# Optimization experiments

Measured on AMD Instinct MI355X. Metric: run time of the kernel, lower is better.

Reference implementation:

```python
import jax, jax.numpy as jnp
import numpy as np

N_STACK = 12
ZERO_OFFSET = 0.001
EPS = 1e-8  # torch cosine_similarity eps


def cos_sim_vec_batch(a, b):
    """torch.cosine_similarity(a[None], b, dim=1): a [V], b [B,V] -> [B]."""
    na = jnp.maximum(jnp.sqrt(jnp.sum(a * a)), EPS)
    nb = jnp.maximum(jnp.sqrt(jnp.sum(b * b, axis=-1)), EPS)
    return (b @ a) / (na * nb)


def setup_inputs() -> dict:
    key = jax.random.key(0)
    k1, k2, k3, k4 = jax.random.split(key, 4)
    B, S, V = 64, 256, 2048
    return {
        "x": jax.random.normal(k1, (B, S, V), dtype=jnp.float32),
        "latch_init": jax.random.normal(k2, (B, V), dtype=jnp.float32),
        "should_pop": jax.random.normal(k3, (V,), dtype=jnp.float32),
        "sharpen_pointer": jnp.ones((1,), dtype=jnp.float32) * 5.0,
        "latch_enable": jax.random.normal(k4, (V,), dtype=jnp.float32) * 0.01,
    }


def reference(x, latch_init, should_pop, sharpen_pointer, latch_enable):
    B, S, V = x.shape
    sharpen = sharpen_pointer[0]
    # Stack state: stack [B, N, V] filled with zero_offset, pointer one-hot at slot 0.
    stack0 = jnp.full((B, N_STACK, V), ZERO_OFFSET, dtype=x.dtype)
    pointer0 = jnp.zeros((B, N_STACK), dtype=x.dtype).at[:, 0].set(1.0)

    def step(carry, inp):
        stack, pointer, latch = carry
        # per-step latch gating -> pop strength (dropout p=0.02 is identity in eval)
        pop = jax.nn.elu(cos_sim_vec_batch(should_pop, latch))  # [B]
        push = 1.0 - pop
        nop = jnp.zeros_like(pop)
        # sharpen the pointer, read the value that would be popped
        psharp = jax.nn.softmax(pointer * sharpen, axis=1)           # [B, N]
        pop_val = jnp.einsum('bnv,bn->bv', stack, psharp)
        # push branch: advance pointer, write value at new top
        push_p = jnp.roll(psharp, 1, axis=1)
        push_stack = stack * (1.0 - push_p[..., None]) + inp[:, None, :] * push_p[..., None]
        # pop branch: erase top back to zero_offset, retreat pointer
        pop_p = jnp.roll(psharp, -1, axis=1)
        pop_stack = stack * (1.0 - psharp[..., None]) + ZERO_OFFSET * psharp[..., None]
        # superposition of the three ops weighted by (push, pop, nop)
        new_stack = (push[:, None, None] * push_stack
                     + pop[:, None, None] * pop_stack
                     + nop[:, None, None] * stack)
        new_pointer = (push[:, None] * push_p
                       + pop[:, None] * pop_p
                       + nop[:, None] * psharp)
        # read stack top, gate by pop strength
        top = jnp.einsum('bnv,bn->bv', new_stack, new_pointer)      # [B, V]
        out = pop[:, None] * top
        # DataLatch update: interp by cosine sim of enable param with enable input
        e = cos_sim_vec_batch(latch_enable, inp)                     # [B]
        new_latch = (1.0 - e)[:, None] * latch + e[:, None] * inp
        return (new_stack, new_pointer, new_latch), (out, new_latch, pop, top)

    x_t = jnp.swapaxes(x, 0, 1)  # [S, B, V]
    _, (outs, latches, pops, tops) = jax.lax.scan(step, (stack0, pointer0, latch_init), x_t)
    outputs = jnp.swapaxes(outs, 0, 1)       # [B, S, V]
    latch_states = jnp.swapaxes(latches, 0, 1)
    pops_out = jnp.swapaxes(pops, 0, 1)       # [B, S]
    stack_tops = jnp.swapaxes(tops, 0, 1)
    return outputs, latch_states, pops_out, stack_tops
```

## Files before the change

kernel.cpp:

```cpp
#include <hip/hip_runtime.h>
#include <math.h>

#define B_ 64
#define S_ 256
#define V_ 2048
#define NS 12
#define ZOFF 0.001f
#define EPSF 1e-8f
#define EPS2 1e-16f
#define NCHS 32

#define WS_NSP2 0
#define WS_D0   64
#define WS_N0   128
#define WS_E    256
#define WS_R    (WS_E + B_*S_)
#define WS_NX2  (WS_R + B_*S_)
#define WS_H    (WS_NX2 + B_*S_)
#define WS_COEF (WS_H + B_*NCHS*S_*4)

typedef float f32x4 __attribute__((ext_vector_type(4)));

template<int CTRL>
__device__ __forceinline__ float dpp_mov(float x) {
    return __int_as_float(__builtin_amdgcn_update_dpp(
        0, __float_as_int(x), CTRL, 0xf, 0xf, true));
}

__device__ __forceinline__ float row16_sum(float x) {
    x += dpp_mov<0x121>(x);
    x += dpp_mov<0x122>(x);
    x += dpp_mov<0x124>(x);
    x += dpp_mov<0x128>(x);
    return x;
}

__device__ __forceinline__ float wave_sum64_fast(float x) {
    x = row16_sum(x);
    x += __shfl_xor(x, 16);
    x += __shfl_xor(x, 32);
    return x;
}

__device__ __forceinline__ void ntstore4(float* p, f32x4 v) {
    __builtin_nontemporal_store(v, (f32x4*)p);
}

__global__ void __launch_bounds__(256) k_e(const float* __restrict__ x,
                                           const float* __restrict__ le,
                                           const float* __restrict__ sp,
                                           const float* __restrict__ l0,
                                           float* __restrict__ ws) {
    int blk = blockIdx.x;
    int tid = threadIdx.x;
    int wave = tid >> 6, lane = tid & 63;
    __shared__ float red4[4][4];
    if (blk >= B_ * S_) {
        int nb = blk - B_ * S_;
        float a = 0.f, b = 0.f;
        if (nb == 0) {
            for (int i = tid; i < V_; i += 256) { float y = sp[i]; a += y * y; }
        } else {
            const float* lr = l0 + (size_t)(nb - 1) * V_;
            for (int i = tid; i < V_; i += 256) {
                float l = lr[i], s = sp[i];
                a += s * l; b += l * l;
            }
        }
        a = wave_sum64_fast(a); b = wave_sum64_fast(b);
        if (lane == 0) { red4[wave][0] = a; red4[wave][1] = b; }
        __syncthreads();
        if (tid == 0) {
            float s0 = red4[0][0] + red4[1][0] + red4[2][0] + red4[3][0];
            float s1 = red4[0][1] + red4[1][1] + red4[2][1] + red4[3][1];
            if (nb == 0) ws[WS_NSP2] = s0;
            else { ws[WS_D0 + nb - 1] = s0; ws[WS_N0 + nb - 1] = s1; }
        }
        return;
    }
    int bt = blk;
    const float4* xb = (const float4*)(x + (size_t)bt * V_);
    const float4* le4 = (const float4*)le;
    const float4* sp4 = (const float4*)sp;
    float dot = 0.f, nx = 0.f, rr = 0.f, nle = 0.f;
#pragma unroll
    for (int k = 0; k < 2; k++) {
        int i = tid + k * 256;
        float4 xv = xb[i], lv = le4[i], sv = sp4[i];
        dot += xv.x * lv.x + xv.y * lv.y + xv.z * lv.z + xv.w * lv.w;
        nx  += xv.x * xv.x + xv.y * xv.y + xv.z * xv.z + xv.w * xv.w;
        rr  += xv.x * sv.x + xv.y * sv.y + xv.z * sv.z + xv.w * sv.w;
        nle += lv.x * lv.x + lv.y * lv.y + lv.z * lv.z + lv.w * lv.w;
    }
    dot = wave_sum64_fast(dot); nx = wave_sum64_fast(nx);
    rr = wave_sum64_fast(rr);   nle = wave_sum64_fast(nle);
    if (lane == 0) {
        red4[wave][0] = dot; red4[wave][1] = nx;
        red4[wave][2] = rr;  red4[wave][3] = nle;
    }
    __syncthreads();
    if (tid == 0) {
        float d  = red4[0][0] + red4[1][0] + red4[2][0] + red4[3][0];
        float n  = red4[0][1] + red4[1][1] + red4[2][1] + red4[3][1];
        float r  = red4[0][2] + red4[1][2] + red4[2][2] + red4[3][2];
        float nl = red4[0][3] + red4[1][3] + red4[2][3] + red4[3][3];
        ws[WS_E + bt]   = d * __frsqrt_rn(fmaxf(nl, EPS2)) * __frsqrt_rn(fmaxf(n, EPS2));
        ws[WS_R + bt]   = r;
        ws[WS_NX2 + bt] = n;
    }
}

__global__ void __launch_bounds__(64) k_latch(const float* __restrict__ x,
                        const float* __restrict__ latch_init,
                        float* __restrict__ latch_out,
                        float* __restrict__ ws) {
    int c = blockIdx.x, b = blockIdx.y;
    int lane = threadIdx.x;
    int v = c * 64 + lane;

    __shared__ float se[S_];
    for (int t = lane; t < S_; t += 64) se[t] = ws[WS_E + b * S_ + t];
    __syncthreads();

    float latch = latch_init[(size_t)b * V_ + v];
    const float* xb = x + (size_t)b * S_ * V_ + v;
    float* lo = latch_out + (size_t)b * S_ * V_ + v;
    float* hpp = ws + WS_H + (size_t)(b * NCHS + c) * S_ * 4;
    bool hwr = (lane & 15) == 0;
    int hq = lane >> 4;

    auto step = [&](int t, float xv, float e) {
        float rs = row16_sum(latch * xv);
        if (hwr) hpp[t * 4 + hq] = rs;
        latch = fmaf(e, xv - latch, latch);
        __builtin_nontemporal_store(latch, lo + (size_t)t * V_);
    };

    float xc[8]; float ec[8];
#pragma unroll
    for (int k = 0; k < 8; k++) { xc[k] = xb[(size_t)k * V_]; ec[k] = se[k]; }
    for (int t = 0; t < S_; t += 8) {
        float y[8], f[8];
        if (t + 8 < S_) {
#pragma unroll
            for (int k = 0; k < 8; k++) {
                y[k] = xb[(size_t)(t + 8 + k) * V_];
                f[k] = se[t + 8 + k];
            }
        } else {
#pragma unroll
            for (int k = 0; k < 8; k++) { y[k] = 0.f; f[k] = 0.f; }
        }
#pragma unroll
        for (int k = 0; k < 8; k++) step(t + k, xc[k], ec[k]);
#pragma unroll
        for (int k = 0; k < 8; k++) { xc[k] = y[k]; ec[k] = f[k]; }
    }
}

template<bool UP>
__device__ __forceinline__ void ptr_fused(int lane, float kq, float inv_nsp,
                                          float d, float n,
                                          const float* __restrict__ se_,
                                          const float* __restrict__ sr_,
                                          const float* __restrict__ snx_,
                                          const float* __restrict__ sh,
                                          float* __restrict__ coef,
                                          float* __restrict__ pops_b) {
    bool act = lane < NS, is0 = (lane == 0), is11 = (lane == 11);
    bool wr = lane <= NS;
    float p = is0 ? 1.f : 0.f;

    float e8[8], r8[8], h8[8], x8[8];
#pragma unroll
    for (int k = 0; k < 8; k++) {
        e8[k] = se_[k]; r8[k] = sr_[k]; h8[k] = sh[k]; x8[k] = snx_[k];
    }
    for (int t = 0; t < S_; t += 8) {
        float e9[8], r9[8], h9[8], x9[8];
        if (t + 8 < S_) {
#pragma unroll
            for (int k = 0; k < 8; k++) {
                e9[k] = se_[t + 8 + k]; r9[k] = sr_[t + 8 + k];
                h9[k] = sh[t + 8 + k];  x9[k] = snx_[t + 8 + k];
            }
        } else {
#pragma unroll
            for (int k = 0; k < 8; k++) { e9[k] = r9[k] = h9[k] = x9[k] = 0.f; }
        }
#pragma unroll
        for (int k = 0; k < 8; k++) {
            float cs = d * inv_nsp * __frsqrt_rn(fmaxf(n, EPS2));
            float pop = cs > 0.f ? cs : __expf(cs) - 1.f;
            float push = 1.f - pop;
            float ez = act ? exp2f(p * kq) : 0.f;
            float s = row16_sum(ez);
            float psh = ez * __frcp_rn(s);
            float fm = UP ? dpp_mov<0x12F>(psh) : dpp_mov<0x121>(psh);
            float fp = UP ? dpp_mov<0x121>(psh) : dpp_mov<0x12F>(psh);
            float wm = UP ? dpp_mov<0x12B>(psh) : dpp_mov<0x125>(psh);
            float wp = UP ? dpp_mov<0x125>(psh) : dpp_mov<0x12B>(psh);
            float push_p = is0  ? wm : fm;
            float pop_p  = is11 ? wp : fp;
            float bb = push * push_p;
            float cc = pop * psh;
            float a  = 1.f - bb - cc;
            float pnew = fmaf(pop, pop_p, bb);
            float4 cv = act ? make_float4(a, bb, cc * ZOFF, pnew)
                            : make_float4(pop, 0.f, 0.f, 0.f);
            if (wr) *(float4*)(coef + (size_t)((t + k) * 13 + lane) * 4) = cv;
            if (lane == 0) pops_b[t + k] = pop;
            p = pnew;
            float e = e8[k], om = 1.f - e;
            d = fmaf(om, d, e * r8[k]);
            n = fmaf(om * om, n, fmaf(2.f * e * om, h8[k], e * e * x8[k]));
        }
#pragma unroll
        for (int k = 0; k < 8; k++) { e8[k] = e9[k]; r8[k] = r9[k]; h8[k] = h9[k]; x8[k] = x9[k]; }
    }
}

__global__ void __launch_bounds__(64) k_ptr(const float* __restrict__ sharpen_ptr,
                                            float* __restrict__ ws,
                                            float* __restrict__ pops_out) {
    int b = blockIdx.x, lane = threadIdx.x;
    __shared__ float sh[S_], se_[S_], sr_[S_], snx_[S_];
    const float4* hp4 = (const float4*)(ws + WS_H) + (size_t)b * NCHS * S_;
    for (int t = lane; t < S_; t += 64) {
        float h = 0.f;
#pragma unroll
        for (int c = 0; c < NCHS; c++) {
            float4 vv = hp4[(size_t)c * S_ + t];
            h += (vv.x + vv.y) + (vv.z + vv.w);
        }
        sh[t] = h;
        se_[t]  = ws[WS_E + b * S_ + t];
        sr_[t]  = ws[WS_R + b * S_ + t];
        snx_[t] = ws[WS_NX2 + b * S_ + t];
    }
    __syncthreads();

    float kq = sharpen_ptr[0] * 1.44269504f;
    float inv_nsp = 1.f / fmaxf(sqrtf(ws[WS_NSP2]), EPSF);
    float d0 = ws[WS_D0 + b];
    float n0 = ws[WS_N0 + b];
    float* coef = ws + WS_COEF + (size_t)b * S_ * 13 * 4;
    float* pops_b = pops_out + (size_t)b * S_;

    float pw = dpp_mov<0x121>((float)lane);
    bool up = (__builtin_amdgcn_readlane(__float_as_int(pw), 0) == __float_as_int(1.0f));
    if (up) ptr_fused<true>(lane, kq, inv_nsp, d0, n0, se_, sr_, snx_, sh, coef, pops_b);
    else    ptr_fused<false>(lane, kq, inv_nsp, d0, n0, se_, sr_, snx_, sh, coef, pops_b);
}

__global__ void __launch_bounds__(128) k_stack(const float* __restrict__ x,
                                               const float* __restrict__ ws,
                                               float* __restrict__ outputs,
                                               float* __restrict__ tops) {
    int b = blockIdx.y, ch = blockIdx.x;
    int tid = threadIdx.x;
    __shared__ float sc[S_ * 52];
    const float4* cb4 = (const float4*)(ws + WS_COEF + (size_t)b * S_ * 52);
    float4* sc4 = (float4*)sc;
    for (int i = tid; i < S_ * 13; i += 128) sc4[i] = cb4[i];
    __syncthreads();

    int v = ch * 512 + tid * 4;
    const float* xp = x + (size_t)b * S_ * V_ + v;
    float* op = outputs + (size_t)b * S_ * V_ + v;
    float* tp = tops + (size_t)b * S_ * V_ + v;

    f32x4 st[NS];
#pragma unroll
    for (int n = 0; n < NS; n++) st[n] = (f32x4){ZOFF, ZOFF, ZOFF, ZOFF};

    auto dstep = [&](int t, f32x4 xv) {
        const float* cf = &sc[t * 52];
        f32x4 top = (f32x4){0.f, 0.f, 0.f, 0.f};
#pragma unroll
        for (int n = 0; n < NS; n++) {
            float4 c4 = *(const float4*)(cf + n * 4);
            f32x4 bx;
            bx.x = fmaf(c4.y, xv.x, c4.z);
            bx.y = fmaf(c4.y, xv.y, c4.z);
            bx.z = fmaf(c4.y, xv.z, c4.z);
            bx.w = fmaf(c4.y, xv.w, c4.z);
            st[n].x = fmaf(c4.x, st[n].x, bx.x);
            st[n].y = fmaf(c4.x, st[n].y, bx.y);
            st[n].z = fmaf(c4.x, st[n].z, bx.z);
            st[n].w = fmaf(c4.x, st[n].w, bx.w);
            top.x = fmaf(c4.w, st[n].x, top.x);
            top.y = fmaf(c4.w, st[n].y, top.y);
            top.z = fmaf(c4.w, st[n].z, top.z);
            top.w = fmaf(c4.w, st[n].w, top.w);
        }
        float pop = cf[48];
        ntstore4(tp + (size_t)t * V_, top);
        f32x4 ot = {pop * top.x, pop * top.y, pop * top.z, pop * top.w};
        ntstore4(op + (size_t)t * V_, ot);
    };

    f32x4 xc[8];
#pragma unroll
    for (int k = 0; k < 8; k++) xc[k] = *(const f32x4*)(xp + (size_t)k * V_);
    for (int t = 0; t < S_; t += 8) {
        f32x4 y[8];
        if (t + 8 < S_) {
#pragma unroll
            for (int k = 0; k < 8; k++) y[k] = *(const f32x4*)(xp + (size_t)(t + 8 + k) * V_);
        } else {
#pragma unroll
            for (int k = 0; k < 8; k++) y[k] = (f32x4){0.f, 0.f, 0.f, 0.f};
        }
#pragma unroll
        for (int k = 0; k < 8; k++) dstep(t + k, xc[k]);
#pragma unroll
        for (int k = 0; k < 8; k++) xc[k] = y[k];
    }
}

extern "C" void kernel_launch(void* const* d_in, const int* in_sizes, int n_in,
                              void* d_out, int out_size, void* d_ws, size_t ws_size,
                              hipStream_t stream) {
    const float* x           = (const float*)d_in[0];
    const float* latch_init  = (const float*)d_in[1];
    const float* should_pop  = (const float*)d_in[2];
    const float* sharpen_ptr = (const float*)d_in[3];
    const float* latch_en    = (const float*)d_in[4];

    float* out = (float*)d_out;
    const size_t BSV = (size_t)B_ * S_ * V_;
    float* outputs      = out;
    float* latch_states = out + BSV;
    float* pops         = out + 2 * BSV;
    float* tops         = out + 2 * BSV + (size_t)B_ * S_;
    float* ws = (float*)d_ws;

    k_e<<<B_ * S_ + 1 + B_, 256, 0, stream>>>(x, latch_en, should_pop, latch_init, ws);
    k_latch<<<dim3(NCHS, B_), 64, 0, stream>>>(x, latch_init, latch_states, ws);
    k_ptr<<<B_, 64, 0, stream>>>(sharpen_ptr, ws, pops);
    k_stack<<<dim3(4, B_), 128, 0, stream>>>(x, ws, outputs, tops);
}
```

Before: 202.2 us.

## Fuse pointer recurrence into stack scan kernel, recomputing coefficients per wave

Removes the separate pointer kernel and the workspace coefficient buffer. Each wave now computes the pointer/pop recurrence step-by-step and writes coefficients to a small double-buffered LDS slot consumed by its own stack scan. This eliminates a launch, the serial single-wave-per-batch phase, and the global round trip for coefficients. In exchange, the serial chain is recomputed redundantly by all 8 waves per batch and lengthens each streaming step's dependency chain.

```diff
diff --git a/kernel.cpp b/kernel.cpp
--- a/kernel.cpp
+++ b/kernel.cpp
@@ -17,7 +17,6 @@
 #define WS_R    (WS_E + B_*S_)
 #define WS_NX2  (WS_R + B_*S_)
 #define WS_H    (WS_NX2 + B_*S_)
-#define WS_COEF (WS_H + B_*NCHS*S_*4)
 
 typedef float f32x4 __attribute__((ext_vector_type(4)));
 
@@ -159,140 +158,67 @@
 }
 
 template<bool UP>
-__device__ __forceinline__ void ptr_fused(int lane, float kq, float inv_nsp,
-                                          float d, float n,
-                                          const float* __restrict__ se_,
-                                          const float* __restrict__ sr_,
-                                          const float* __restrict__ snx_,
-                                          const float* __restrict__ sh,
-                                          float* __restrict__ coef,
-                                          float* __restrict__ pops_b) {
+__device__ __forceinline__ void fused_loop(
+    int lane, float kq, float inv_nsp, float d, float n,
+    const float* __restrict__ sh, const float* __restrict__ se_,
+    const float* __restrict__ sr_, const float* __restrict__ snx_,
+    float* __restrict__ slot0, float* __restrict__ slot1,
+    const float* __restrict__ xp, float* __restrict__ op,
+    float* __restrict__ tp, float* __restrict__ pops_b, bool wrpops)
+{
     bool act = lane < NS, is0 = (lane == 0), is11 = (lane == 11);
-    bool wr = lane <= NS;
     float p = is0 ? 1.f : 0.f;
 
-    float e8[8], r8[8], h8[8], x8[8];
-#pragma unroll
-    for (int k = 0; k < 8; k++) {
-        e8[k] = se_[k]; r8[k] = sr_[k]; h8[k] = sh[k]; x8[k] = snx_[k];
-    }
-    for (int t = 0; t < S_; t += 8) {
-        float e9[8], r9[8], h9[8], x9[8];
-        if (t + 8 < S_) {
-#pragma unroll
-            for (int k = 0; k < 8; k++) {
-                e9[k] = se_[t + 8 + k]; r9[k] = sr_[t + 8 + k];
-                h9[k] = sh[t + 8 + k];  x9[k] = snx_[t + 8 + k];
-            }
-        } else {
-#pragma unroll
-            for (int k = 0; k < 8; k++) { e9[k] = r9[k] = h9[k] = x9[k] = 0.f; }
-        }
-#pragma unroll
-        for (int k = 0; k < 8; k++) {
-            float cs = d * inv_nsp * __frsqrt_rn(fmaxf(n, EPS2));
-            float pop = cs > 0.f ? cs : __expf(cs) - 1.f;
-            float push = 1.f - pop;
-            float ez = act ? exp2f(p * kq) : 0.f;
-            float s = row16_sum(ez);
-            float psh = ez * __frcp_rn(s);
-            float fm = UP ? dpp_mov<0x12F>(psh) : dpp_mov<0x121>(psh);
-            float fp = UP ? dpp_mov<0x121>(psh) : dpp_mov<0x12F>(psh);
-            float wm = UP ? dpp_mov<0x12B>(psh) : dpp_mov<0x125>(psh);
-            float wp = UP ? dpp_mov<0x125>(psh) : dpp_mov<0x12B>(psh);
-            float push_p = is0  ? wm : fm;
-            float pop_p  = is11 ? wp : fp;
-            float bb = push * push_p;
-            float cc = pop * psh;
-            float a  = 1.f - bb - cc;
-            float pnew = fmaf(pop, pop_p, bb);
-            float4 cv = act ? make_float4(a, bb, cc * ZOFF, pnew)
-                            : make_float4(pop, 0.f, 0.f, 0.f);
-            if (wr) *(float4*)(coef + (size_t)((t + k) * 13 + lane) * 4) = cv;
-            if (lane == 0) pops_b[t + k] = pop;
-            p = pnew;
-            float e = e8[k], om = 1.f - e;
-            d = fmaf(om, d, e * r8[k]);
-            n = fmaf(om * om, n, fmaf(2.f * e * om, h8[k], e * e * x8[k]));
-        }
-#pragma unroll
-        for (int k = 0; k < 8; k++) { e8[k] = e9[k]; r8[k] = r9[k]; h8[k] = h9[k]; x8[k] = x9[k]; }
-    }
-}
-
-__global__ void __launch_bounds__(64) k_ptr(const float* __restrict__ sharpen_ptr,
-                                            float* __restrict__ ws,
-                                            float* __restrict__ pops_out) {
-    int b = blockIdx.x, lane = threadIdx.x;
-    __shared__ float sh[S_], se_[S_], sr_[S_], snx_[S_];
-    const float4* hp4 = (const float4*)(ws + WS_H) + (size_t)b * NCHS * S_;
-    for (int t = lane; t < S_; t += 64) {
-        float h = 0.f;
-#pragma unroll
-        for (int c = 0; c < NCHS; c++) {
-            float4 vv = hp4[(size_t)c * S_ + t];
-            h += (vv.x + vv.y) + (vv.z + vv.w);
-        }
-        sh[t] = h;
-        se_[t]  = ws[WS_E + b * S_ + t];
-        sr_[t]  = ws[WS_R + b * S_ + t];
-        snx_[t] = ws[WS_NX2 + b * S_ + t];
-    }
-    __syncthreads();
-
-    float kq = sharpen_ptr[0] * 1.44269504f;
-    float inv_nsp = 1.f / fmaxf(sqrtf(ws[WS_NSP2]), EPSF);
-    float d0 = ws[WS_D0 + b];
-    float n0 = ws[WS_N0 + b];
-    float* coef = ws + WS_COEF + (size_t)b * S_ * 13 * 4;
-    float* pops_b = pops_out + (size_t)b * S_;
-
-    float pw = dpp_mov<0x121>((float)lane);
-    bool up = (__builtin_amdgcn_readlane(__float_as_int(pw), 0) == __float_as_int(1.0f));
-    if (up) ptr_fused<true>(lane, kq, inv_nsp, d0, n0, se_, sr_, snx_, sh, coef, pops_b);
-    else    ptr_fused<false>(lane, kq, inv_nsp, d0, n0, se_, sr_, snx_, sh, coef, pops_b);
-}
-
-__global__ void __launch_bounds__(128) k_stack(const float* __restrict__ x,
-                                               const float* __restrict__ ws,
-                                               float* __restrict__ outputs,
-                                               float* __restrict__ tops) {
-    int b = blockIdx.y, ch = blockIdx.x;
-    int tid = threadIdx.x;
-    __shared__ float sc[S_ * 52];
-    const float4* cb4 = (const float4*)(ws + WS_COEF + (size_t)b * S_ * 52);
-    float4* sc4 = (float4*)sc;
-    for (int i = tid; i < S_ * 13; i += 128) sc4[i] = cb4[i];
-    __syncthreads();
-
-    int v = ch * 512 + tid * 4;
-    const float* xp = x + (size_t)b * S_ * V_ + v;
-    float* op = outputs + (size_t)b * S_ * V_ + v;
-    float* tp = tops + (size_t)b * S_ * V_ + v;
+    auto chain_step = [&](int t, float* slot) {
+        float e = se_[t], r = sr_[t], hh = sh[t], xx = snx_[t];
+        float cs = d * inv_nsp * __frsqrt_rn(fmaxf(n, EPS2));
+        float pop = cs > 0.f ? cs : __expf(cs) - 1.f;
+        float push = 1.f - pop;
+        float ez = act ? exp2f(p * kq) : 0.f;
+        float s = row16_sum(ez);
+        float psh = ez * __frcp_rn(s);
+        float fm = UP ? dpp_mov<0x12F>(psh) : dpp_mov<0x121>(psh);
+        float fp = UP ? dpp_mov<0x121>(psh) : dpp_mov<0x12F>(psh);
+        float wm = UP ? dpp_mov<0x12B>(psh) : dpp_mov<0x125>(psh);
+        float wp = UP ? dpp_mov<0x125>(psh) : dpp_mov<0x12B>(psh);
+        float push_p = is0  ? wm : fm;
+        float pop_p  = is11 ? wp : fp;
+        float bb = push * push_p;
+        float cc = pop * psh;
+        float a  = 1.f - bb - cc;
+        float pnew = fmaf(pop, pop_p, bb);
+        float4 cv = act ? make_float4(a, bb, cc * ZOFF, pnew)
+                        : make_float4(pop, 0.f, 0.f, 0.f);
+        if (lane <= NS) *(float4*)(slot + lane * 4) = cv;
+        if (wrpops && lane == 0) pops_b[t] = pop;
+        p = pnew;
+        float om = 1.f - e;
+        d = fmaf(om, d, e * r);
+        n = fmaf(om * om, n, fmaf(2.f * e * om, hh, e * e * xx));
+    };
 
     f32x4 st[NS];
 #pragma unroll
-    for (int n = 0; n < NS; n++) st[n] = (f32x4){ZOFF, ZOFF, ZOFF, ZOFF};
-
-    auto dstep = [&](int t, f32x4 xv) {
-        const float* cf = &sc[t * 52];
+    for (int i = 0; i < NS; i++) st[i] = (f32x4){ZOFF, ZOFF, ZOFF, ZOFF};
+
+    auto scan_step = [&](const float* cf, int t, f32x4 xv) {
         f32x4 top = (f32x4){0.f, 0.f, 0.f, 0.f};
 #pragma unroll
-        for (int n = 0; n < NS; n++) {
-            float4 c4 = *(const float4*)(cf + n * 4);
+        for (int i = 0; i < NS; i++) {
+            float4 c4 = *(const float4*)(cf + i * 4);
             f32x4 bx;
             bx.x = fmaf(c4.y, xv.x, c4.z);
             bx.y = fmaf(c4.y, xv.y, c4.z);
             bx.z = fmaf(c4.y, xv.z, c4.z);
             bx.w = fmaf(c4.y, xv.w, c4.z);
-            st[n].x = fmaf(c4.x, st[n].x, bx.x);
-            st[n].y = fmaf(c4.x, st[n].y, bx.y);
-            st[n].z = fmaf(c4.x, st[n].z, bx.z);
-            st[n].w = fmaf(c4.x, st[n].w, bx.w);
-            top.x = fmaf(c4.w, st[n].x, top.x);
-            top.y = fmaf(c4.w, st[n].y, top.y);
-            top.z = fmaf(c4.w, st[n].z, top.z);
-            top.w = fmaf(c4.w, st[n].w, top.w);
+            st[i].x = fmaf(c4.x, st[i].x, bx.x);
+            st[i].y = fmaf(c4.x, st[i].y, bx.y);
+            st[i].z = fmaf(c4.x, st[i].z, bx.z);
+            st[i].w = fmaf(c4.x, st[i].w, bx.w);
+            top.x = fmaf(c4.w, st[i].x, top.x);
+            top.y = fmaf(c4.w, st[i].y, top.y);
+            top.z = fmaf(c4.w, st[i].z, top.z);
+            top.w = fmaf(c4.w, st[i].w, top.w);
         }
         float pop = cf[48];
         ntstore4(tp + (size_t)t * V_, top);
@@ -300,6 +226,7 @@
         ntstore4(op + (size_t)t * V_, ot);
     };
 
+    chain_step(0, slot0);
     f32x4 xc[8];
 #pragma unroll
     for (int k = 0; k < 8; k++) xc[k] = *(const f32x4*)(xp + (size_t)k * V_);
@@ -313,10 +240,61 @@
             for (int k = 0; k < 8; k++) y[k] = (f32x4){0.f, 0.f, 0.f, 0.f};
         }
 #pragma unroll
-        for (int k = 0; k < 8; k++) dstep(t + k, xc[k]);
+        for (int k = 0; k < 8; k++) {
+            int tt = t + k;
+            if (tt + 1 < S_) chain_step(tt + 1, ((tt + 1) & 1) ? slot1 : slot0);
+            scan_step((tt & 1) ? slot1 : slot0, tt, xc[k]);
+        }
 #pragma unroll
         for (int k = 0; k < 8; k++) xc[k] = y[k];
     }
+}
+
+__global__ void __launch_bounds__(128) k_stackptr(const float* __restrict__ sharpen_ptr,
+                                                  const float* __restrict__ x,
+                                                  float* __restrict__ ws,
+                                                  float* __restrict__ pops_out,
+                                                  float* __restrict__ outputs,
+                                                  float* __restrict__ tops) {
+    int b = blockIdx.y, ch = blockIdx.x;
+    int tid = threadIdx.x;
+    int w = tid >> 6, lane = tid & 63;
+    __shared__ float sh[S_], se_[S_], sr_[S_], snx_[S_];
+    __shared__ float scoef[2][2][52];
+
+    const float4* hp4 = (const float4*)(ws + WS_H) + (size_t)b * NCHS * S_;
+    for (int t = tid; t < S_; t += 128) {
+        float h = 0.f;
+#pragma unroll
+        for (int c = 0; c < NCHS; c++) {
+            float4 vv = hp4[(size_t)c * S_ + t];
+            h += (vv.x + vv.y) + (vv.z + vv.w);
+        }
+        sh[t] = h;
+        se_[t]  = ws[WS_E + b * S_ + t];
+        sr_[t]  = ws[WS_R + b * S_ + t];
+        snx_[t] = ws[WS_NX2 + b * S_ + t];
+    }
+    __syncthreads();
+
+    float kq = sharpen_ptr[0] * 1.44269504f;
+    float inv_nsp = 1.f / fmaxf(sqrtf(ws[WS_NSP2]), EPSF);
+    float d0 = ws[WS_D0 + b];
+    float n0 = ws[WS_N0 + b];
+
+    int v = ch * 512 + w * 256 + lane * 4;
+    const float* xp = x + (size_t)b * S_ * V_ + v;
+    float* op = outputs + (size_t)b * S_ * V_ + v;
+    float* tp = tops + (size_t)b * S_ * V_ + v;
+    float* pops_b = pops_out + (size_t)b * S_;
+    bool wrpops = (ch == 0 && w == 0);
+
+    float pw = dpp_mov<0x121>((float)lane);
+    bool up = (__builtin_amdgcn_readlane(__float_as_int(pw), 0) == __float_as_int(1.0f));
+    if (up) fused_loop<true>(lane, kq, inv_nsp, d0, n0, sh, se_, sr_, snx_,
+                             &scoef[w][0][0], &scoef[w][1][0], xp, op, tp, pops_b, wrpops);
+    else    fused_loop<false>(lane, kq, inv_nsp, d0, n0, sh, se_, sr_, snx_,
+                              &scoef[w][0][0], &scoef[w][1][0], xp, op, tp, pops_b, wrpops);
 }
 
 extern "C" void kernel_launch(void* const* d_in, const int* in_sizes, int n_in,
@@ -338,6 +316,5 @@
 
     k_e<<<B_ * S_ + 1 + B_, 256, 0, stream>>>(x, latch_en, should_pop, latch_init, ws);
     k_latch<<<dim3(NCHS, B_), 64, 0, stream>>>(x, latch_init, latch_states, ws);
-    k_ptr<<<B_, 64, 0, stream>>>(sharpen_ptr, ws, pops);
-    k_stack<<<dim3(4, B_), 128, 0, stream>>>(x, ws, outputs, tops);
-}
+    k_stackptr<<<dim3(4, B_), 128, 0, stream>>>(sharpen_ptr, x, ws, pops, outputs, tops);
+}
```

Measured after the change: 197.1 us. 1.03x faster.
